# Kernel tuning notes

Measured on AMD Instinct MI355X. Metric: run time of the kernel, lower is better.

## Reference

```python
import jax, jax.numpy as jnp
import numpy as np

INPUT_DIM = 8192
HIDDEN = 512
EMBED = HIDDEN // 2  # op embedding dim
NUM_TEMPERS = 64
NUM_OPS = 3
MAX_HOPS = 4
B = 2048


def setup_inputs() -> dict:
    key = jax.random.key(0)
    ks = jax.random.split(key, 10)
    n = lambda k, shape: jax.random.normal(k, shape, jnp.float32)
    return {
        "x": n(ks[0], (B, INPUT_DIM)),
        "op_emb": 0.01 * n(ks[1], (NUM_OPS, EMBED)),
        "op_logits": jnp.zeros((NUM_OPS,), jnp.float32),
        "id_embeds": 0.01 * n(ks[2], (128, 4)),
        "W1": n(ks[3], (HIDDEN + 4 + EMBED, HIDDEN)) / np.sqrt(HIDDEN + 4 + EMBED),
        "b1": jnp.zeros((HIDDEN,), jnp.float32),
        "W2": n(ks[4], (HIDDEN, HIDDEN)) / np.sqrt(HIDDEN),
        "b2": jnp.zeros((HIDDEN,), jnp.float32),
        "Wr1": n(ks[5], (HIDDEN + 4, 32)) / np.sqrt(HIDDEN + 4),
        "br1": jnp.zeros((32,), jnp.float32),
        "Wr2": n(ks[6], (32, NUM_TEMPERS + 1)) / np.sqrt(32),
        "br2": jnp.zeros((NUM_TEMPERS + 1,), jnp.float32),
        "Wp": n(ks[7], (HIDDEN, INPUT_DIM)) / np.sqrt(HIDDEN),
        "bp": jnp.zeros((INPUT_DIM,), jnp.float32),
        "tid_emb": 0.01 * n(ks[8], (NUM_TEMPERS, 4)),
        "rng_seed": 42,
    }


def reference(x, op_emb, op_logits, id_embeds, W1, b1, W2, b2, Wr1, br1, Wr2, br2, Wp, bp, tid_emb, rng_seed):
    Bx, D = x.shape
    # D is a multiple of HIDDEN here -> no padding branch needed
    num_patches = D // HIDDEN
    patch_states = x.reshape(Bx * num_patches, HIDDEN)
    N = patch_states.shape[0]

    rng = jax.random.key(rng_seed)
    rng, tk = jax.random.split(rng)
    patch_tempers = jax.random.randint(tk, (N,), 0, NUM_TEMPERS)
    patch_done = jnp.zeros((N,), bool)

    # Fixed-length unroll of the while_loop (max_hops=4). Early-exit only
    # differs if ALL patches stop early, which is vanishingly unlikely.
    for hop in range(MAX_HOPS):
        # --- gather active patches (inactive slots fill with index 0, as in original) ---
        active_idx = jnp.where(~patch_done, size=N, fill_value=0)[0]
        x_active = patch_states[active_idx]          # [N, HIDDEN]
        t_active = patch_tempers[active_idx]         # [N]
        # --- Temper: sample op per patch, embed, 2-layer relu MLP ---
        rng, ok = jax.random.split(rng)
        op_probs = jax.nn.softmax(op_logits)
        op_idx = jax.random.categorical(ok, jnp.log(op_probs), shape=(N,))
        x_aug = jnp.concatenate([x_active, id_embeds[t_active], op_emb[op_idx]], axis=-1)
        h = jax.nn.relu(x_aug @ W1 + b1)
        h = jax.nn.relu(h @ W2 + b2)                 # [N, HIDDEN]
        # --- scatter back updated states ---
        patch_states = patch_states.at[active_idx].set(h)
        # --- routing policy + categorical sampling of next temper / stop ---
        enriched = jnp.concatenate([h, tid_emb[t_active]], axis=-1)
        logits = jax.nn.relu(enriched @ Wr1 + br1) @ Wr2 + br2
        rng, sk = jax.random.split(rng)
        sampled = jax.random.categorical(sk, jax.nn.log_softmax(logits))
        stop = sampled == NUM_TEMPERS
        next_t = jnp.clip(sampled, 0, NUM_TEMPERS - 1)
        patch_tempers = patch_tempers.at[active_idx].set(next_t)
        patch_done = patch_done.at[active_idx].set(stop)

    latent = patch_states.reshape(Bx, num_patches, HIDDEN).mean(axis=1)  # [B, HIDDEN]
    pred = latent @ Wp + bp                                              # [B, INPUT_DIM]
    return latent, pred
```

## Files before the change

kernel.cpp:

```cpp
#include <hip/hip_runtime.h>
#include <cstdint>
#include <cstddef>


#define NPATCH 32768
#define NHOP 4
#define RSCALE 4096.0f
#define RINV   2.44140625e-4f

typedef unsigned short u16;
typedef __attribute__((ext_vector_type(8))) _Float16 half8;
typedef __attribute__((ext_vector_type(4))) float f32x4;

#define GLDS(gp, lp) __builtin_amdgcn_global_load_lds( \
    (const __attribute__((address_space(1))) void*)(const void*)(gp), \
    (__attribute__((address_space(3))) void*)(void*)(lp), 16, 0, 0)

__device__ __forceinline__ uint32_t rotl32(uint32_t x, int r){ return (x<<r)|(x>>(32-r)); }

__device__ __forceinline__ void tf2x32(uint32_t k0, uint32_t k1, uint32_t x0, uint32_t x1,
                                       uint32_t& o0, uint32_t& o1){
  uint32_t k2 = k0 ^ k1 ^ 0x1BD11BDAu;
  x0 += k0; x1 += k1;
#define TFR(r) { x0 += x1; x1 = rotl32(x1,(r)); x1 ^= x0; }
  TFR(13) TFR(15) TFR(26) TFR(6)   x0 += k1; x1 += k2 + 1u;
  TFR(17) TFR(29) TFR(16) TFR(24)  x0 += k2; x1 += k0 + 2u;
  TFR(13) TFR(15) TFR(26) TFR(6)   x0 += k0; x1 += k1 + 3u;
  TFR(17) TFR(29) TFR(16) TFR(24)  x0 += k1; x1 += k2 + 4u;
  TFR(13) TFR(15) TFR(26) TFR(6)   x0 += k2; x1 += k0 + 5u;
#undef TFR
  o0 = x0; o1 = x1;
}

__device__ __forceinline__ uint32_t jbits32(uint32_t k0, uint32_t k1, uint32_t idx){
  uint32_t a, b; tf2x32(k0, k1, 0u, idx, a, b);
  return a ^ b;
}

__device__ __forceinline__ void jsplit(uint32_t& r0, uint32_t& r1, uint32_t& c0, uint32_t& c1){
  uint32_t n0, n1;
  tf2x32(r0, r1, 0u, 0u, n0, n1);
  tf2x32(r0, r1, 0u, 1u, c0, c1);
  r0 = n0; r1 = n1;
}

__device__ __forceinline__ float jgumbel(uint32_t bits){
  float f = __uint_as_float(0x3f800000u | (bits >> 9)) - 1.0f;
  float u = fmaxf(f, 1.17549435e-38f);
  return -logf(-logf(u));
}

union uhcv { _Float16 h; u16 u; };
__device__ __forceinline__ u16 f2h(float x){ uhcv t; t.h = (_Float16)x; return t.u; }
__device__ __forceinline__ float h2f(u16 b){ uhcv t; t.u = b; return (float)t.h; }
__device__ __forceinline__ void split2s(float v, u16& a0, u16& a1){
  a0 = f2h(v);
  a1 = f2h((v - h2f(a0)) * RSCALE);
}

__global__ void k_keys(const int* __restrict__ seed, const float* __restrict__ op_logits,
                       uint32_t* __restrict__ keys, float* __restrict__ logp3){
  if (threadIdx.x != 0 || blockIdx.x != 0) return;
  uint32_t r0 = 0u, r1 = (uint32_t)seed[0];
  uint32_t c0, c1;
  jsplit(r0, r1, c0, c1); keys[0] = c0; keys[1] = c1;
  for (int h = 0; h < NHOP; h++){
    jsplit(r0, r1, c0, c1); keys[2 + 4*h] = c0; keys[3 + 4*h] = c1;
    jsplit(r0, r1, c0, c1); keys[4 + 4*h] = c0; keys[5 + 4*h] = c1;
  }
  float l0 = op_logits[0], l1 = op_logits[1], l2 = op_logits[2];
  float mm = fmaxf(l0, fmaxf(l1, l2));
  float e0 = expf(l0-mm), e1 = expf(l1-mm), e2 = expf(l2-mm);
  float ssum = e0 + e1 + e2;
  logp3[0] = logf(e0/ssum); logp3[1] = logf(e1/ssum); logp3[2] = logf(e2/ssum);
}

__global__ __launch_bounds__(256)
void k_init(const uint32_t* __restrict__ keys, int* __restrict__ tempers, int* __restrict__ done){
  int i = blockIdx.x*256 + threadIdx.x;
  uint32_t b = jbits32(keys[0], keys[1], (uint32_t)(NPATCH + i));
  tempers[i] = (int)(b & 63u);
  done[i] = 0;
}

__global__ __launch_bounds__(256)
void k_precomp(const float* __restrict__ id_embeds, const float* __restrict__ op_emb,
               const float* __restrict__ tid_emb,
               const float* __restrict__ W1, const float* __restrict__ b1,
               const float* __restrict__ Wr1, const float* __restrict__ br1,
               float* __restrict__ idW, float* __restrict__ opWb, float* __restrict__ tidWb){
  int b = blockIdx.x, tid = threadIdx.x;
  if (b < 64){
    for (int j = tid; j < 512; j += 256){
      float v = 0.f;
      #pragma unroll
      for (int u = 0; u < 4; u++) v = fmaf(id_embeds[b*4+u], W1[(size_t)(512+u)*512 + j], v);
      idW[b*512 + j] = v;
    }
  } else if (b < 67){
    int o = b - 64;
    for (int j = tid; j < 512; j += 256){
      float v = b1[j];
      for (int u = 0; u < 256; u++) v = fmaf(op_emb[o*256+u], W1[(size_t)(516+u)*512 + j], v);
      opWb[o*512 + j] = v;
    }
  } else {
    for (int idx = tid; idx < 2048; idx += 256){
      int t = idx >> 5, c = idx & 31;
      float v = br1[c];
      #pragma unroll
      for (int u = 0; u < 4; u++) v = fmaf(tid_emb[t*4+u], Wr1[(512+u)*32 + c], v);
      tidWb[idx] = v;
    }
  }
}

__global__ __launch_bounds__(256)
void k_splitW(const float* __restrict__ W1, const float* __restrict__ W2,
              const float* __restrict__ Wp, const float* __restrict__ Wr1,
              u16* __restrict__ W1T, u16* __restrict__ W2T, u16* __restrict__ WpT,
              u16* __restrict__ Wr1P){
  __shared__ float t[32][33];
  int blk = blockIdx.x;
  const float* src; u16* dst; int N; int deg; size_t pst; int tb;
  if (blk < 256){ src = W1; dst = W1T; N = 512; deg = 2; pst = (size_t)512*512; tb = blk; }
  else if (blk < 512){ src = W2; dst = W2T; N = 512; deg = 2; pst = (size_t)512*512; tb = blk - 256; }
  else if (blk < 528){ src = Wr1; dst = Wr1P; N = 32; deg = 2; pst = (size_t)32*512; tb = blk - 512; }
  else { src = Wp; dst = WpT; N = 8192; deg = 1; pst = 0; tb = blk - 528; }
  int n0 = (tb >> 4)*32, k0 = (tb & 15)*32;
  if (N == 32){ n0 = 0; k0 = tb*32; }
  int r = threadIdx.x >> 5, c = threadIdx.x & 31;
  for (int rr = r; rr < 32; rr += 8)
    t[rr][c] = src[(size_t)(k0+rr)*N + ((n0 + c) % N)];
  __syncthreads();
  for (int rr = r; rr < 32; rr += 8){
    if (n0 + rr >= N) break;
    float v = t[c][rr];
    size_t o = (size_t)(n0+rr)*512 + k0 + c;
    if (deg == 2){
      u16 a0, a1; split2s(v, a0, a1);
      dst[o] = a0; dst[pst + o] = a1;
    } else {
      dst[o] = f2h(v);
    }
  }
}

__global__ __launch_bounds__(256)
void k_xsplit(const float* __restrict__ x, u16* __restrict__ sP){
  size_t i = ((size_t)blockIdx.x*256 + threadIdx.x)*4;
  float4 v = *(const float4*)(x + i);
  ushort4 p0, p1;
  split2s(v.x, p0.x, p1.x); split2s(v.y, p0.y, p1.y);
  split2s(v.z, p0.z, p1.z); split2s(v.w, p0.w, p1.w);
  const size_t SP = (size_t)NPATCH*512;
  *(ushort4*)(sP + i) = p0; *(ushort4*)(sP + SP + i) = p1;
}

__global__ __launch_bounds__(1024)
void k_scan1(const int* __restrict__ done, int* __restrict__ lpref,
             int* __restrict__ partials){
  __shared__ int cnt[1024];
  const int tid = threadIdx.x;
  const int e = blockIdx.x*1024 + tid;
  int f = (done[e] == 0);
  cnt[tid] = f;
  __syncthreads();
  int val = f;
  for (int off = 1; off < 1024; off <<= 1){
    int v = (tid >= off) ? cnt[tid - off] : 0;
    __syncthreads();
    val += v; cnt[tid] = val;
    __syncthreads();
  }
  lpref[e] = val - f;
  if (tid == 1023) partials[blockIdx.x] = val;
}

__global__ void k_scan2(int* __restrict__ partials, int* __restrict__ meta){
  const int tid = threadIdx.x;
  int f = (tid < 32) ? partials[tid] : 0;
  int v = f;
  #pragma unroll
  for (int off = 1; off < 32; off <<= 1){
    int u = __shfl_up(v, off);
    if (tid >= off) v += u;
  }
  if (tid < 32) partials[tid] = v - f;
  if (tid == 31){
    meta[0] = v;
    meta[1] = (v < NPATCH) ? (NPATCH - 1) : 0;
  }
}

__global__ __launch_bounds__(1024)
void k_scan3(const int* __restrict__ done, const int* __restrict__ lpref,
             const int* __restrict__ partials, const int* __restrict__ meta,
             const int* __restrict__ tempers,
             const uint32_t* __restrict__ keys, const float* __restrict__ logp3,
             int hop, int* __restrict__ aidx, int* __restrict__ t_act,
             int* __restrict__ op_idx){
  const int tid = threadIdx.x;
  const int e = blockIdx.x*1024 + tid;
  const int base = partials[blockIdx.x];
  const int lp = lpref[e];
  const int f = (done[e] == 0);
  const int na = meta[0];
  const int pos = f ? (base + lp) : (na + (e - base - lp));
  const int p = f ? e : 0;
  aidx[pos] = p;
  t_act[pos] = tempers[p];
  const uint32_t k0 = keys[2 + 4*hop], k1 = keys[3 + 4*hop];
  float best = 0.f; int bi = 0;
  #pragma unroll
  for (int c = 0; c < 3; c++){
    float v = jgumbel(jbits32(k0, k1, (uint32_t)(3*pos + c))) + logp3[c];
    if (c == 0 || v > best){ best = v; bi = c; }
  }
  op_idx[pos] = bi;
}

__global__ __launch_bounds__(1024)
void k_scan(const int* __restrict__ done, int* __restrict__ aidx, int* __restrict__ meta){
  __shared__ int cnt[1024];
  int tid = threadIdx.x;
  int base = tid * 32;
  unsigned flags = 0; int c = 0;
  #pragma unroll
  for (int i = 0; i < 32; i++){
    int f = (done[base + i] == 0);
    flags |= ((unsigned)f) << i;
    c += f;
  }
  cnt[tid] = c;
  __syncthreads();
  int val = c;
  for (int off = 1; off < 1024; off <<= 1){
    int v = (tid >= off) ? cnt[tid - off] : 0;
    __syncthreads();
    val += v; cnt[tid] = val;
    __syncthreads();
  }
  int pos = val - c;
  for (int i = 0; i < 32; i++){
    if ((flags >> i) & 1u) aidx[pos++] = base + i;
  }
  __syncthreads();
  int na = cnt[1023];
  for (int j = na + tid; j < NPATCH; j += 1024) aidx[j] = 0;
  if (tid == 0){
    meta[0] = na;
    meta[1] = (na < NPATCH) ? (NPATCH - 1) : 0;
  }
}

__global__ __launch_bounds__(256)
void k_gather(const int* __restrict__ aidx, const int* __restrict__ tempers,
              const uint32_t* __restrict__ keys, const float* __restrict__ logp3,
              int hop, int* __restrict__ t_act, int* __restrict__ op_idx){
  int s = blockIdx.x*256 + threadIdx.x;
  int p = aidx[s];
  t_act[s] = tempers[p];
  uint32_t k0 = keys[2 + 4*hop], k1 = keys[3 + 4*hop];
  float best = 0.f; int bi = 0;
  #pragma unroll
  for (int c = 0; c < 3; c++){
    float v = jgumbel(jbits32(k0, k1, (uint32_t)(3*s + c))) + logp3[c];
    if (c == 0 || v > best){ best = v; bi = c; }
  }
  op_idx[s] = bi;
}

template<int MODE, int DEG>
__global__ __launch_bounds__(256, 2)
void k_mgemm(const u16* __restrict__ Ap, const u16* __restrict__ Bp,
             float* __restrict__ outF, u16* __restrict__ outP,
             const int* __restrict__ aidx, const float* __restrict__ bias,
             const float* __restrict__ idW, const float* __restrict__ opWb,
             const int* __restrict__ t_act, const int* __restrict__ op_idx,
             const int* __restrict__ meta,
             int Ncols, size_t aStride, size_t bStride, size_t oStride){
  __shared__ u16 As[2*DEG*4096];
  __shared__ u16 Bs[2*DEG*4096];
  const int tid = threadIdx.x;
  const int L = tid & 63, w = tid >> 6;

  const int gx = (int)gridDim.x;
  const int nwg = gx * (int)gridDim.y;
  int lin = (int)blockIdx.y * gx + (int)blockIdx.x;
  if ((nwg & 7) == 0)
    lin = (lin & 7) * (nwg >> 3) + (lin >> 3);
  const int m0 = (lin / gx) * 128, n0 = (lin % gx) * 128;
  const int wr = w >> 1, wc = w & 1;

  constexpr int SPW = DEG*4;
  constexpr int BUFO = DEG*4096;
  const bool isA = (w < 2);
  const u16* gB = isA ? Ap : Bp;
  u16* lB = isA ? As : Bs;
  const size_t pstride = isA ? aStride : bStride;
  const u16* gseg[8];
  u16* lseg[8];
  #pragma unroll
  for (int q = 0; q < SPW; q++){
    int ss = (w & 1)*SPW + q;
    int p = ss >> 3, rb = ss & 7;
    int row16 = rb*16 + (L >> 2);
    int grow;
    if (isA) grow = (MODE == 1) ? aidx[m0 + row16] : (m0 + row16);
    else     grow = n0 + row16;
    int swz = (L & 3) ^ ((L >> 2) & 3);
    gseg[q] = gB + p*pstride + (size_t)grow*512 + swz*8;
    lseg[q] = lB + p*4096 + rb*512;
  }

  f32x4 accM[4][4], accR[4][4];
  #pragma unroll
  for (int i = 0; i < 4; i++)
    #pragma unroll
    for (int j = 0; j < 4; j++){ accM[i][j] = (f32x4)0.f; accR[i][j] = (f32x4)0.f; }

  const int rdsw = ((L >> 4) ^ (L & 3))*8;
  const int frow = L & 15;

  #pragma unroll
  for (int q = 0; q < SPW; q++)
    GLDS(gseg[q], lseg[q]);

  #pragma unroll 2
  for (int kt = 0; kt < 16; kt++){
    const int cb = (kt & 1) * BUFO;
    if (kt < 15){
      const int nb = ((kt + 1) & 1) * BUFO;
      #pragma unroll
      for (int q = 0; q < SPW; q++)
        GLDS(gseg[q] + (kt+1)*32, lseg[q] + nb);
      asm volatile("s_waitcnt vmcnt(%0)" :: "n"(SPW) : "memory");
    } else {
      asm volatile("s_waitcnt vmcnt(0)" ::: "memory");
    }
    __builtin_amdgcn_s_barrier();
    asm volatile("" ::: "memory");

    __builtin_amdgcn_s_setprio(1);
    #pragma unroll
    for (int pa = 0; pa < DEG; pa++){
      half8 af[4];
      #pragma unroll
      for (int i = 0; i < 4; i++)
        af[i] = *(const half8*)&As[cb + pa*4096 + (wr*64 + i*16 + frow)*32 + rdsw];
      #pragma unroll
      for (int pb = 0; pb < DEG - pa; pb++){
        #pragma unroll
        for (int j = 0; j < 4; j++){
          half8 bf = *(const half8*)&Bs[cb + pb*4096 + (wc*64 + j*16 + frow)*32 + rdsw];
          #pragma unroll
          for (int i = 0; i < 4; i++){
            if (pa + pb == 0)
              accM[i][j] = __builtin_amdgcn_mfma_f32_16x16x32_f16(af[i], bf, accM[i][j], 0, 0, 0);
            else
              accR[i][j] = __builtin_amdgcn_mfma_f32_16x16x32_f16(af[i], bf, accR[i][j], 0, 0, 0);
          }
        }
      }
    }
    __builtin_amdgcn_s_setprio(0);

    asm volatile("" ::: "memory");
    __builtin_amdgcn_s_barrier();
  }

  const int rbase = m0 + wr*64 + (L >> 4)*4;
  const int cbase = n0 + wc*64 + (L & 15);
  const int w0v = (MODE == 3) ? meta[1] : 0;
  #pragma unroll
  for (int i = 0; i < 4; i++){
    #pragma unroll
    for (int reg = 0; reg < 4; reg++){
      int r = rbase + i*16 + reg;
      if (MODE == 1){
        int t = t_act[r], o = op_idx[r];
        #pragma unroll
        for (int j = 0; j < 4; j++){
          int c = cbase + j*16;
          float v = accM[i][j][reg] + RINV*accR[i][j][reg] + idW[t*512 + c] + opWb[o*512 + c];
          v = fmaxf(v, 0.f);
          u16 a0, a1; split2s(v, a0, a1);
          size_t off = (size_t)r*512 + c;
          outP[off] = a0; outP[oStride + off] = a1;
        }
      } else if (MODE == 3){
        int p = aidx[r];
        bool allowed = (p != 0) || (r == w0v);
        #pragma unroll
        for (int j = 0; j < 4; j++){
          int c = cbase + j*16;
          float v = accM[i][j][reg] + RINV*accR[i][j][reg] + bias[c];
          v = fmaxf(v, 0.f);
          if (allowed){
            u16 a0, a1; split2s(v, a0, a1);
            size_t off = (size_t)p*512 + c;
            outP[off] = a0; outP[oStride + off] = a1;
          }
        }
      } else {
        #pragma unroll
        for (int j = 0; j < 4; j++){
          int c = cbase + j*16;
          float v = accM[i][j][reg] + bias[c];
          if (DEG == 2) v += RINV*accR[i][j][reg];
          outF[(size_t)r*Ncols + c] = v;
        }
      }
    }
  }
}

__global__ __launch_bounds__(256)
void k_routemm(const u16* __restrict__ sP, const u16* __restrict__ Wr1P,
               const int* __restrict__ aidx, const int* __restrict__ t_act,
               const float* __restrict__ tidWb, float* __restrict__ l32g){
  const int tid = threadIdx.x;
  const int L = tid & 63, w = tid >> 6;
  const int s0 = blockIdx.x*64 + w*16;
  const size_t SPh = (size_t)NPATCH*512;

  const int arow = aidx[s0 + (L & 15)];
  const u16* a0p = sP + (size_t)arow*512 + (L >> 4)*8;
  const u16* a1p = a0p + SPh;
  const u16* bb = Wr1P + (size_t)(L & 15)*512 + (L >> 4)*8;
  const size_t BPL = (size_t)32*512;
  const size_t BCT = (size_t)16*512;

  f32x4 accM[2], accR[2];
  accM[0] = (f32x4)0.f; accM[1] = (f32x4)0.f;
  accR[0] = (f32x4)0.f; accR[1] = (f32x4)0.f;

  #pragma unroll 4
  for (int kt = 0; kt < 16; kt++){
    const int ko = kt*32;
    half8 a0  = *(const half8*)(a0p + ko);
    half8 a1  = *(const half8*)(a1p + ko);
    half8 b00 = *(const half8*)(bb + ko);
    half8 b01 = *(const half8*)(bb + BCT + ko);
    half8 b10 = *(const half8*)(bb + BPL + ko);
    half8 b11 = *(const half8*)(bb + BPL + BCT + ko);
    accM[0] = __builtin_amdgcn_mfma_f32_16x16x32_f16(a0, b00, accM[0], 0, 0, 0);
    accM[1] = __builtin_amdgcn_mfma_f32_16x16x32_f16(a0, b01, accM[1], 0, 0, 0);
    accR[0] = __builtin_amdgcn_mfma_f32_16x16x32_f16(a0, b10, accR[0], 0, 0, 0);
    accR[1] = __builtin_amdgcn_mfma_f32_16x16x32_f16(a0, b11, accR[1], 0, 0, 0);
    accR[0] = __builtin_amdgcn_mfma_f32_16x16x32_f16(a1, b00, accR[0], 0, 0, 0);
    accR[1] = __builtin_amdgcn_mfma_f32_16x16x32_f16(a1, b01, accR[1], 0, 0, 0);
  }

  #pragma unroll
  for (int reg = 0; reg < 4; reg++){
    int s = s0 + (L >> 4)*4 + reg;
    int t = t_act[s];
    #pragma unroll
    for (int ct = 0; ct < 2; ct++){
      int c = ct*16 + (L & 15);
      float v = accM[ct][reg] + RINV*accR[ct][reg] + tidWb[t*32 + c];
      l32g[(size_t)s*32 + c] = fmaxf(v, 0.f);
    }
  }
}

__global__ __launch_bounds__(256)
void k_sample(const float* __restrict__ l32g, const float* __restrict__ Wr2,
              const float* __restrict__ br2,
              const int* __restrict__ aidx, const int* __restrict__ meta,
              const uint32_t* __restrict__ keys, int hop,
              int* __restrict__ tempers, int* __restrict__ done){
  __shared__ float l32s[8][32];
  __shared__ float Wr2s[32*65];
  const int tid = threadIdx.x;
  const int s0 = blockIdx.x * 8;
  l32s[tid >> 5][tid & 31] = l32g[(size_t)s0*32 + tid];
  for (int i = tid; i < 32*65; i += 256) Wr2s[i] = Wr2[i];
  __syncthreads();

  const int lane = tid & 63, w = tid >> 6;
  const int half = lane >> 5;
  const uint32_t sk0 = keys[4 + 4*hop], sk1 = keys[5 + 4*hop];
  int smp[2];
  for (int pass = 0; pass < 2; pass++){
    const int psl = w*2 + pass;
    const int ps  = s0 + psl;
    const int c = lane;
    float lg = br2[c];
    #pragma unroll
    for (int k = 0; k < 32; k++) lg = fmaf(l32s[psl][k], Wr2s[k*65 + c], lg);
    float lg64 = br2[64];
    #pragma unroll
    for (int k = 0; k < 32; k++) lg64 = fmaf(l32s[psl][k], Wr2s[k*65 + 64], lg64);
    float m = lg;
    for (int off = 32; off; off >>= 1) m = fmaxf(m, __shfl_xor(m, off));
    m = fmaxf(m, lg64);
    float se = expf(lg - m);
    for (int off = 32; off; off >>= 1) se += __shfl_xor(se, off);
    se += expf(lg64 - m);
    float Lse = logf(se);
    float g = jgumbel(jbits32(sk0, sk1, (uint32_t)(65*ps + c)));
    float v = (lg - m) - Lse + g;
    int idx = c;
    for (int off = 32; off; off >>= 1){
      float ov = __shfl_xor(v, off);
      int   oi = __shfl_xor(idx, off);
      if (ov > v || (ov == v && oi < idx)){ v = ov; idx = oi; }
    }
    float g64 = jgumbel(jbits32(sk0, sk1, (uint32_t)(65*ps + 64)));
    float v64 = (lg64 - m) - Lse + g64;
    if (v64 > v) idx = 64;
    smp[pass] = idx;
  }

  const int s = s0 + w*2 + half;
  const int mysmp = smp[half];
  const int p = aidx[s];
  const bool allowed = (p != 0) || (s == meta[1]);
  if (allowed && (lane & 31) == 0){
    tempers[p] = (mysmp < 63) ? mysmp : 63;
    done[p]    = (mysmp == 64) ? 1 : 0;
  }
}

__global__ __launch_bounds__(256)
void k_latent2(const u16* __restrict__ sP, float* __restrict__ outF, u16* __restrict__ latP){
  int idx = blockIdx.x*256 + threadIdx.x;
  int b = idx >> 9, j = idx & 511;
  const size_t SP = (size_t)NPATCH*512;
  float s = 0.f;
  #pragma unroll 4
  for (int u = 0; u < 16; u++){
    size_t e = (size_t)(b*16 + u)*512 + j;
    s += h2f(sP[e]) + RINV*h2f(sP[SP + e]);
  }
  s *= 0.0625f;
  outF[idx] = s;
  latP[idx] = f2h(s);
}

template<int MODE>
__global__ __launch_bounds__(256)
void k_gemmF(const float* __restrict__ A, const float* __restrict__ B, float* __restrict__ C,
             int Ncols,
             const int* __restrict__ aidx,
             const float* __restrict__ bias,
             const float* __restrict__ idW, const float* __restrict__ opWb,
             const int* __restrict__ t_act, const int* __restrict__ op_idx){
  __shared__ float As[16][128];
  __shared__ float Bs[16][128];
  const int tid = threadIdx.x;
  const int bx = blockIdx.x, by = blockIdx.y;
  const int tx = tid & 15, ty = tid >> 4;
  const int lr = tid >> 1, lhalf = tid & 1;
  const int srow = by*128 + lr;
  const int arow = (MODE == 1) ? aidx[srow] : srow;
  const float* Ap = A + (size_t)arow*512 + lhalf*8;
  const float* Bp = B + (size_t)(tid >> 4)*Ncols + bx*128 + (tid & 15)*8;

  float acc[8][8];
  #pragma unroll
  for (int i = 0; i < 8; i++)
    #pragma unroll
    for (int j = 0; j < 8; j++) acc[i][j] = 0.f;

  for (int kt = 0; kt < 512; kt += 16){
    float4 a0 = *(const float4*)(Ap + kt);
    float4 a1 = *(const float4*)(Ap + kt + 4);
    float4 g0 = *(const float4*)(Bp + (size_t)kt*Ncols);
    float4 g1 = *(const float4*)(Bp + (size_t)kt*Ncols + 4);
    __syncthreads();
    As[lhalf*8+0][lr] = a0.x; As[lhalf*8+1][lr] = a0.y;
    As[lhalf*8+2][lr] = a0.z; As[lhalf*8+3][lr] = a0.w;
    As[lhalf*8+4][lr] = a1.x; As[lhalf*8+5][lr] = a1.y;
    As[lhalf*8+6][lr] = a1.z; As[lhalf*8+7][lr] = a1.w;
    *(float4*)&Bs[tid>>4][(tid&15)*8]     = g0;
    *(float4*)&Bs[tid>>4][(tid&15)*8 + 4] = g1;
    __syncthreads();
    #pragma unroll
    for (int k = 0; k < 16; k++){
      float4 av0 = *(float4*)&As[k][ty*8];
      float4 av1 = *(float4*)&As[k][ty*8+4];
      float4 bv0 = *(float4*)&Bs[k][tx*4];
      float4 bv1 = *(float4*)&Bs[k][64 + tx*4];
      float av[8] = {av0.x,av0.y,av0.z,av0.w,av1.x,av1.y,av1.z,av1.w};
      float bv[8] = {bv0.x,bv0.y,bv0.z,bv0.w,bv1.x,bv1.y,bv1.z,bv1.w};
      #pragma unroll
      for (int i = 0; i < 8; i++)
        #pragma unroll
        for (int j = 0; j < 8; j++)
          acc[i][j] = fmaf(av[i], bv[j], acc[i][j]);
    }
  }

  const int col0a = bx*128 + tx*4;
  const int col0b = col0a + 64;
  #pragma unroll
  for (int i = 0; i < 8; i++){
    int s = by*128 + ty*8 + i;
    float adda[4], addb[4];
    if (MODE == 1){
      int t = t_act[s], o = op_idx[s];
      float4 ia = *(const float4*)&idW[t*512 + col0a];
      float4 ib = *(const float4*)&idW[t*512 + col0b];
      float4 oa = *(const float4*)&opWb[o*512 + col0a];
      float4 ob = *(const float4*)&opWb[o*512 + col0b];
      adda[0]=ia.x+oa.x; adda[1]=ia.y+oa.y; adda[2]=ia.z+oa.z; adda[3]=ia.w+oa.w;
      addb[0]=ib.x+ob.x; addb[1]=ib.y+ob.y; addb[2]=ib.z+ob.z; addb[3]=ib.w+ob.w;
    } else {
      float4 ba = *(const float4*)&bias[col0a];
      float4 bb = *(const float4*)&bias[col0b];
      adda[0]=ba.x; adda[1]=ba.y; adda[2]=ba.z; adda[3]=ba.w;
      addb[0]=bb.x; addb[1]=bb.y; addb[2]=bb.z; addb[3]=bb.w;
    }
    float4 va, vb;
    float* pa = &va.x; float* pb = &vb.x;
    #pragma unroll
    for (int j = 0; j < 4; j++){
      float v0 = acc[i][j]   + adda[j];
      float v1 = acc[i][j+4] + addb[j];
      if (MODE != 2){ v0 = fmaxf(v0, 0.f); v1 = fmaxf(v1, 0.f); }
      pa[j] = v0; pb[j] = v1;
    }
    *(float4*)(C + (size_t)s*Ncols + col0a) = va;
    *(float4*)(C + (size_t)s*Ncols + col0b) = vb;
  }
}

__global__ __launch_bounds__(256)
void k_routeF(const float* __restrict__ h2, const float* __restrict__ Wr1,
              const float* __restrict__ Wr2, const float* __restrict__ br2,
              const float* __restrict__ tidWb,
              const int* __restrict__ t_act, const int* __restrict__ aidx,
              const int* __restrict__ meta, const uint32_t* __restrict__ keys, int hop,
              float* __restrict__ states, int* __restrict__ tempers, int* __restrict__ done){
  __shared__ float Wr1s[256][32];
  __shared__ float h2s[8][512];
  __shared__ float l32[8][32];

  const int tid = threadIdx.x;
  const int s0 = blockIdx.x * 8;

  for (int i4 = tid; i4 < 8*128; i4 += 256){
    int sl = i4 >> 7, q = i4 & 127;
    *(float4*)&h2s[sl][q*4] = *(const float4*)&h2[(size_t)(s0+sl)*512 + q*4];
  }

  const int lane = tid & 63, w = tid >> 6;
  const int half = lane >> 5, col = lane & 31;
  const int sl = w*2 + half;
  const int s  = s0 + sl;
  const int t  = t_act[s];
  float acc = tidWb[t*32 + col];

  for (int kh = 0; kh < 2; kh++){
    __syncthreads();
    for (int idx = tid; idx < 256*32; idx += 256)
      Wr1s[idx >> 5][idx & 31] = Wr1[kh*8192 + idx];
    __syncthreads();
    const int kb = kh * 256;
    #pragma unroll 4
    for (int k4 = 0; k4 < 64; k4++){
      float4 hv = *(float4*)&h2s[sl][kb + k4*4];
      acc = fmaf(hv.x, Wr1s[k4*4+0][col], acc);
      acc = fmaf(hv.y, Wr1s[k4*4+1][col], acc);
      acc = fmaf(hv.z, Wr1s[k4*4+2][col], acc);
      acc = fmaf(hv.w, Wr1s[k4*4+3][col], acc);
    }
  }
  l32[sl][col] = fmaxf(acc, 0.f);
  __syncthreads();

  const uint32_t sk0 = keys[4 + 4*hop], sk1 = keys[5 + 4*hop];
  int smp[2];
  for (int pass = 0; pass < 2; pass++){
    const int psl = w*2 + pass;
    const int ps  = s0 + psl;
    const int c = lane;
    float lg = br2[c];
    #pragma unroll
    for (int k = 0; k < 32; k++) lg = fmaf(l32[psl][k], Wr2[k*65 + c], lg);
    float lg64 = br2[64];
    #pragma unroll
    for (int k = 0; k < 32; k++) lg64 = fmaf(l32[psl][k], Wr2[k*65 + 64], lg64);
    float m = lg;
    for (int off = 32; off; off >>= 1) m = fmaxf(m, __shfl_xor(m, off));
    m = fmaxf(m, lg64);
    float se = expf(lg - m);
    for (int off = 32; off; off >>= 1) se += __shfl_xor(se, off);
    se += expf(lg64 - m);
    float Lse = logf(se);
    float g = jgumbel(jbits32(sk0, sk1, (uint32_t)(65*ps + c)));
    float v = (lg - m) - Lse + g;
    int idx = c;
    for (int off = 32; off; off >>= 1){
      float ov = __shfl_xor(v, off);
      int   oi = __shfl_xor(idx, off);
      if (ov > v || (ov == v && oi < idx)){ v = ov; idx = oi; }
    }
    float g64 = jgumbel(jbits32(sk0, sk1, (uint32_t)(65*ps + 64)));
    float v64 = (lg64 - m) - Lse + g64;
    if (v64 > v) idx = 64;
    smp[pass] = idx;
  }

  const int mysmp = smp[half];
  const int p = aidx[s];
  const int w0v = meta[1];
  const bool allowed = (p != 0) || (s == w0v);
  if (allowed){
    const float4* src = (const float4*)&h2s[sl][0];
    float4* dst = (float4*)(states + (size_t)p*512);
    for (int q = col; q < 128; q += 32) dst[q] = src[q];
    if (col == 0){
      tempers[p] = (mysmp < 63) ? mysmp : 63;
      done[p]    = (mysmp == 64) ? 1 : 0;
    }
  }
}

__global__ __launch_bounds__(256)
void k_latentF(const float* __restrict__ states, float* __restrict__ out){
  int idx = blockIdx.x*256 + threadIdx.x;
  int b = idx >> 9, j = idx & 511;
  float s = 0.f;
  #pragma unroll
  for (int u = 0; u < 16; u++) s += states[(size_t)(b*16 + u)*512 + j];
  out[idx] = s * 0.0625f;
}

extern "C" void kernel_launch(void* const* d_in, const int* in_sizes, int n_in,
                              void* d_out, int out_size, void* d_ws, size_t ws_size,
                              hipStream_t stream) {
  (void)in_sizes; (void)n_in; (void)out_size;
  const float* x         = (const float*)d_in[0];
  const float* op_emb    = (const float*)d_in[1];
  const float* op_logits = (const float*)d_in[2];
  const float* id_embeds = (const float*)d_in[3];
  const float* W1        = (const float*)d_in[4];
  const float* b1        = (const float*)d_in[5];
  const float* W2        = (const float*)d_in[6];
  const float* b2        = (const float*)d_in[7];
  const float* Wr1       = (const float*)d_in[8];
  const float* br1       = (const float*)d_in[9];
  const float* Wr2       = (const float*)d_in[10];
  const float* br2       = (const float*)d_in[11];
  const float* Wp        = (const float*)d_in[12];
  const float* bp        = (const float*)d_in[13];
  const float* tid_emb   = (const float*)d_in[14];
  const int*   seed      = (const int*)d_in[15];
  float* out = (float*)d_out;

  char* w = (char*)d_ws;
  uint32_t* keys = (uint32_t*)w;
  float* logp3   = (float*)(w + 256);
  int*   meta    = (int*)(w + 512);
  int*   tempers = (int*)(w + 4096);
  int*   done    = tempers + NPATCH;
  int*   t_act   = done + NPATCH;
  int*   op_idx  = t_act + NPATCH;
  int*   aidx    = op_idx + NPATCH;
  int*   lpref   = aidx + NPATCH;
  float* idW     = (float*)(lpref + NPATCH);
  float* opWb    = idW + 64*512;
  float* tidWb   = opWb + 3*512;
  int*   partials= (int*)(tidWb + 2048);

  const size_t SPh = (size_t)NPATCH*512;
  u16* W1T     = (u16*)(w + (1u<<20));
  u16* W2T     = W1T + (size_t)2*512*512;
  u16* Wr1P    = W2T + (size_t)2*512*512;
  u16* WpT     = Wr1P + (size_t)2*32*512;
  u16* latP    = WpT + (size_t)8192*512;
  u16* statesP = latP + (size_t)2048*512;
  u16* h1P     = statesP + 2*SPh;
  float* l32g  = (float*)(h1P + 2*SPh);
  const size_t NEED = (size_t)((char*)(l32g + (size_t)NPATCH*32) - w);

  k_keys<<<1, 64, 0, stream>>>(seed, op_logits, keys, logp3);
  k_init<<<NPATCH/256, 256, 0, stream>>>(keys, tempers, done);
  k_precomp<<<68, 256, 0, stream>>>(id_embeds, op_emb, tid_emb, W1, b1, Wr1, br1,
                                    idW, opWb, tidWb);

  if (ws_size >= NEED){
    k_splitW<<<4624, 256, 0, stream>>>(W1, W2, Wp, Wr1, W1T, W2T, WpT, Wr1P);
    k_xsplit<<<(NPATCH*512/4)/256, 256, 0, stream>>>(x, statesP);

    for (int hop = 0; hop < NHOP; hop++){
      k_scan1<<<NPATCH/1024, 1024, 0, stream>>>(done, lpref, partials);
      k_scan2<<<1, 64, 0, stream>>>(partials, meta);
      k_scan3<<<NPATCH/1024, 1024, 0, stream>>>(done, lpref, partials, meta,
                                                tempers, keys, logp3, hop,
                                                aidx, t_act, op_idx);
      k_mgemm<1,2><<<dim3(4, NPATCH/128), 256, 0, stream>>>(
          statesP, W1T, nullptr, h1P, aidx, nullptr, idW, opWb, t_act, op_idx, meta,
          512, SPh, (size_t)512*512, SPh);
      k_mgemm<3,2><<<dim3(4, NPATCH/128), 256, 0, stream>>>(
          h1P, W2T, nullptr, statesP, aidx, b2, nullptr, nullptr, nullptr, nullptr, meta,
          512, SPh, (size_t)512*512, SPh);
      k_routemm<<<NPATCH/64, 256, 0, stream>>>(statesP, Wr1P, aidx, t_act, tidWb, l32g);
      k_sample<<<NPATCH/8, 256, 0, stream>>>(l32g, Wr2, br2, aidx, meta, keys, hop,
                                             tempers, done);
    }

    k_latent2<<<(2048*512)/256, 256, 0, stream>>>(statesP, out, latP);
    k_mgemm<2,1><<<dim3(64, 16), 256, 0, stream>>>(
        latP, WpT, out + 2048*512, nullptr, nullptr, bp, nullptr, nullptr, nullptr, nullptr,
        nullptr, 8192, (size_t)2048*512, (size_t)8192*512, 0);
  } else {
    const size_t BIG0 = 2u<<20;
    const size_t SB   = (size_t)NPATCH * 512 * sizeof(float);
    float *states, *h1, *h2;
    bool copy_states;
    if (ws_size >= BIG0 + 3*SB){
      states = (float*)(w + BIG0);
      h1     = (float*)(w + BIG0 + SB);
      h2     = (float*)(w + BIG0 + 2*SB);
      copy_states = true;
    } else {
      states = (float*)d_in[0];
      h1     = (float*)(w + BIG0);
      h2     = (float*)(w + BIG0 + SB);
      copy_states = false;
    }
    if (copy_states)
      hipMemcpyAsync(states, x, SB, hipMemcpyDeviceToDevice, stream);

    for (int hop = 0; hop < NHOP; hop++){
      k_scan<<<1, 1024, 0, stream>>>(done, aidx, meta);
      k_gather<<<NPATCH/256, 256, 0, stream>>>(aidx, tempers, keys, logp3, hop, t_act, op_idx);
      k_gemmF<1><<<dim3(4, NPATCH/128), 256, 0, stream>>>(states, W1, h1, 512,
                                      aidx, nullptr, idW, opWb, t_act, op_idx);
      k_gemmF<0><<<dim3(4, NPATCH/128), 256, 0, stream>>>(h1, W2, h2, 512,
                                      nullptr, b2, nullptr, nullptr, nullptr, nullptr);
      k_routeF<<<NPATCH/8, 256, 0, stream>>>(h2, Wr1, Wr2, br2, tidWb, t_act, aidx,
                                      meta, keys, hop, states, tempers, done);
    }

    k_latentF<<<(2048*512)/256, 256, 0, stream>>>(states, out);
    k_gemmF<2><<<dim3(8192/128, 2048/128), 256, 0, stream>>>(out, Wp, out + 2048*512, 8192,
                                      nullptr, bp, nullptr, nullptr, nullptr, nullptr);
  }
}
```

Measured before the change: 985.7 us.

## Fuse scan2 into scan3, fuse route sampling into routemm, vectorize latent

Folds the single-block partial-sum scan into every scan3 block, removing one launch per hop. Merges the sampling kernel into the routing GEMM, so the 32-wide hidden activations stay in shared memory instead of round-tripping through global memory. Restructures the GEMM inner loop to preload all A and B fragments before issuing MFMAs, which raises register use. Vectorizes the latent mean kernel to 4-wide loads and stores. Risks include the larger register footprint and the serialized 16-row sampling loop per wave.

After: 986.0 us. About the same (+0.0%).

```diff
diff --git a/kernel.cpp b/kernel.cpp
--- a/kernel.cpp
+++ b/kernel.cpp
@@ -177,35 +177,32 @@
   if (tid == 1023) partials[blockIdx.x] = val;
 }
 
-__global__ void k_scan2(int* __restrict__ partials, int* __restrict__ meta){
-  const int tid = threadIdx.x;
-  int f = (tid < 32) ? partials[tid] : 0;
-  int v = f;
-  #pragma unroll
-  for (int off = 1; off < 32; off <<= 1){
-    int u = __shfl_up(v, off);
-    if (tid >= off) v += u;
-  }
-  if (tid < 32) partials[tid] = v - f;
-  if (tid == 31){
-    meta[0] = v;
-    meta[1] = (v < NPATCH) ? (NPATCH - 1) : 0;
-  }
-}
-
 __global__ __launch_bounds__(1024)
 void k_scan3(const int* __restrict__ done, const int* __restrict__ lpref,
-             const int* __restrict__ partials, const int* __restrict__ meta,
+             const int* __restrict__ partials,
              const int* __restrict__ tempers,
              const uint32_t* __restrict__ keys, const float* __restrict__ logp3,
              int hop, int* __restrict__ aidx, int* __restrict__ t_act,
-             int* __restrict__ op_idx){
+             int* __restrict__ op_idx, int* __restrict__ meta){
+  __shared__ int sb[33];
   const int tid = threadIdx.x;
+  if (tid < 64){
+    int f = (tid < 32) ? partials[tid] : 0;
+    int v = f;
+    #pragma unroll
+    for (int off = 1; off < 32; off <<= 1){
+      int u = __shfl_up(v, off);
+      if (tid >= off) v += u;
+    }
+    if (tid < 32) sb[tid] = v - f;
+    if (tid == 31) sb[32] = v;
+  }
+  __syncthreads();
+  const int base = sb[blockIdx.x];
+  const int na = sb[32];
   const int e = blockIdx.x*1024 + tid;
-  const int base = partials[blockIdx.x];
   const int lp = lpref[e];
   const int f = (done[e] == 0);
-  const int na = meta[0];
   const int pos = f ? (base + lp) : (na + (e - base - lp));
   const int p = f ? e : 0;
   aidx[pos] = p;
@@ -218,6 +215,10 @@
     if (c == 0 || v > best){ best = v; bi = c; }
   }
   op_idx[pos] = bi;
+  if (blockIdx.x == 0 && tid == 0){
+    meta[0] = na;
+    meta[1] = (na < NPATCH) ? (NPATCH - 1) : 0;
+  }
 }
 
 __global__ __launch_bounds__(1024)
@@ -343,27 +344,30 @@
     asm volatile("" ::: "memory");
 
     __builtin_amdgcn_s_setprio(1);
-    #pragma unroll
-    for (int pa = 0; pa < DEG; pa++){
-      half8 af[4];
+    half8 af[DEG][4], bf[DEG][4];
+    #pragma unroll
+    for (int pa = 0; pa < DEG; pa++)
       #pragma unroll
       for (int i = 0; i < 4; i++)
-        af[i] = *(const half8*)&As[cb + pa*4096 + (wr*64 + i*16 + frow)*32 + rdsw];
+        af[pa][i] = *(const half8*)&As[cb + pa*4096 + (wr*64 + i*16 + frow)*32 + rdsw];
+    #pragma unroll
+    for (int pb = 0; pb < DEG; pb++)
       #pragma unroll
-      for (int pb = 0; pb < DEG - pa; pb++){
+      for (int j = 0; j < 4; j++)
+        bf[pb][j] = *(const half8*)&Bs[cb + pb*4096 + (wc*64 + j*16 + frow)*32 + rdsw];
+    #pragma unroll
+    for (int pa = 0; pa < DEG; pa++)
+      #pragma unroll
+      for (int pb = 0; pb < DEG - pa; pb++)
         #pragma unroll
-        for (int j = 0; j < 4; j++){
-          half8 bf = *(const half8*)&Bs[cb + pb*4096 + (wc*64 + j*16 + frow)*32 + rdsw];
+        for (int j = 0; j < 4; j++)
           #pragma unroll
           for (int i = 0; i < 4; i++){
             if (pa + pb == 0)
-              accM[i][j] = __builtin_amdgcn_mfma_f32_16x16x32_f16(af[i], bf, accM[i][j], 0, 0, 0);
+              accM[i][j] = __builtin_amdgcn_mfma_f32_16x16x32_f16(af[0][i], bf[0][j], accM[i][j], 0, 0, 0);
             else
-              accR[i][j] = __builtin_amdgcn_mfma_f32_16x16x32_f16(af[i], bf, accR[i][j], 0, 0, 0);
+              accR[i][j] = __builtin_amdgcn_mfma_f32_16x16x32_f16(af[pa][i], bf[pb][j], accR[i][j], 0, 0, 0);
           }
-        }
-      }
-    }
     __builtin_amdgcn_s_setprio(0);
 
     asm volatile("" ::: "memory");
@@ -419,11 +423,18 @@
 __global__ __launch_bounds__(256)
 void k_routemm(const u16* __restrict__ sP, const u16* __restrict__ Wr1P,
                const int* __restrict__ aidx, const int* __restrict__ t_act,
-               const float* __restrict__ tidWb, float* __restrict__ l32g){
+               const float* __restrict__ tidWb,
+               const float* __restrict__ Wr2, const float* __restrict__ br2,
+               const int* __restrict__ meta, const uint32_t* __restrict__ keys,
+               int hop, int* __restrict__ tempers, int* __restrict__ done){
+  __shared__ float l32s[64][32];
+  __shared__ float Wr2s[32*65];
   const int tid = threadIdx.x;
   const int L = tid & 63, w = tid >> 6;
   const int s0 = blockIdx.x*64 + w*16;
   const size_t SPh = (size_t)NPATCH*512;
+
+  for (int i = tid; i < 32*65; i += 256) Wr2s[i] = Wr2[i];
 
   const int arow = aidx[s0 + (L & 15)];
   const u16* a0p = sP + (size_t)arow*512 + (L >> 4)*8;
@@ -455,45 +466,30 @@
 
   #pragma unroll
   for (int reg = 0; reg < 4; reg++){
-    int s = s0 + (L >> 4)*4 + reg;
+    int sl = w*16 + (L >> 4)*4 + reg;
+    int s = blockIdx.x*64 + sl;
     int t = t_act[s];
     #pragma unroll
     for (int ct = 0; ct < 2; ct++){
       int c = ct*16 + (L & 15);
       float v = accM[ct][reg] + RINV*accR[ct][reg] + tidWb[t*32 + c];
-      l32g[(size_t)s*32 + c] = fmaxf(v, 0.f);
-    }
-  }
-}
-
-__global__ __launch_bounds__(256)
-void k_sample(const float* __restrict__ l32g, const float* __restrict__ Wr2,
-              const float* __restrict__ br2,
-              const int* __restrict__ aidx, const int* __restrict__ meta,
-              const uint32_t* __restrict__ keys, int hop,
-              int* __restrict__ tempers, int* __restrict__ done){
-  __shared__ float l32s[8][32];
-  __shared__ float Wr2s[32*65];
-  const int tid = threadIdx.x;
-  const int s0 = blockIdx.x * 8;
-  l32s[tid >> 5][tid & 31] = l32g[(size_t)s0*32 + tid];
-  for (int i = tid; i < 32*65; i += 256) Wr2s[i] = Wr2[i];
+      l32s[sl][c] = fmaxf(v, 0.f);
+    }
+  }
   __syncthreads();
 
-  const int lane = tid & 63, w = tid >> 6;
-  const int half = lane >> 5;
   const uint32_t sk0 = keys[4 + 4*hop], sk1 = keys[5 + 4*hop];
-  int smp[2];
-  for (int pass = 0; pass < 2; pass++){
-    const int psl = w*2 + pass;
-    const int ps  = s0 + psl;
-    const int c = lane;
+  const int w0v = meta[1];
+  for (int rr = 0; rr < 16; rr++){
+    const int sl = w*16 + rr;
+    const int ps = blockIdx.x*64 + sl;
+    const int c = L;
     float lg = br2[c];
     #pragma unroll
-    for (int k = 0; k < 32; k++) lg = fmaf(l32s[psl][k], Wr2s[k*65 + c], lg);
+    for (int k = 0; k < 32; k++) lg = fmaf(l32s[sl][k], Wr2s[k*65 + c], lg);
     float lg64 = br2[64];
     #pragma unroll
-    for (int k = 0; k < 32; k++) lg64 = fmaf(l32s[psl][k], Wr2s[k*65 + 64], lg64);
+    for (int k = 0; k < 32; k++) lg64 = fmaf(l32s[sl][k], Wr2s[k*65 + 64], lg64);
     float m = lg;
     for (int off = 32; off; off >>= 1) m = fmaxf(m, __shfl_xor(m, off));
     m = fmaxf(m, lg64);
@@ -512,33 +508,38 @@
     float g64 = jgumbel(jbits32(sk0, sk1, (uint32_t)(65*ps + 64)));
     float v64 = (lg64 - m) - Lse + g64;
     if (v64 > v) idx = 64;
-    smp[pass] = idx;
-  }
-
-  const int s = s0 + w*2 + half;
-  const int mysmp = smp[half];
-  const int p = aidx[s];
-  const bool allowed = (p != 0) || (s == meta[1]);
-  if (allowed && (lane & 31) == 0){
-    tempers[p] = (mysmp < 63) ? mysmp : 63;
-    done[p]    = (mysmp == 64) ? 1 : 0;
+    if (L == 0){
+      const int p = aidx[ps];
+      const bool allowed = (p != 0) || (ps == w0v);
+      if (allowed){
+        tempers[p] = (idx < 63) ? idx : 63;
+        done[p]    = (idx == 64) ? 1 : 0;
+      }
+    }
   }
 }
 
 __global__ __launch_bounds__(256)
 void k_latent2(const u16* __restrict__ sP, float* __restrict__ outF, u16* __restrict__ latP){
   int idx = blockIdx.x*256 + threadIdx.x;
-  int b = idx >> 9, j = idx & 511;
+  int b = idx >> 7, j4 = (idx & 127)*4;
   const size_t SP = (size_t)NPATCH*512;
-  float s = 0.f;
+  float s0 = 0.f, s1 = 0.f, s2 = 0.f, s3 = 0.f;
   #pragma unroll 4
   for (int u = 0; u < 16; u++){
-    size_t e = (size_t)(b*16 + u)*512 + j;
-    s += h2f(sP[e]) + RINV*h2f(sP[SP + e]);
-  }
-  s *= 0.0625f;
-  outF[idx] = s;
-  latP[idx] = f2h(s);
+    size_t e = (size_t)(b*16 + u)*512 + j4;
+    ushort4 v0 = *(const ushort4*)(sP + e);
+    ushort4 v1 = *(const ushort4*)(sP + SP + e);
+    s0 += h2f(v0.x) + RINV*h2f(v1.x);
+    s1 += h2f(v0.y) + RINV*h2f(v1.y);
+    s2 += h2f(v0.z) + RINV*h2f(v1.z);
+    s3 += h2f(v0.w) + RINV*h2f(v1.w);
+  }
+  s0 *= 0.0625f; s1 *= 0.0625f; s2 *= 0.0625f; s3 *= 0.0625f;
+  float4 fo; fo.x = s0; fo.y = s1; fo.z = s2; fo.w = s3;
+  *(float4*)(outF + (size_t)b*512 + j4) = fo;
+  ushort4 lp; lp.x = f2h(s0); lp.y = f2h(s1); lp.z = f2h(s2); lp.w = f2h(s3);
+  *(ushort4*)(latP + (size_t)b*512 + j4) = lp;
 }
 
 template<int MODE>
@@ -776,8 +777,7 @@
   u16* latP    = WpT + (size_t)8192*512;
   u16* statesP = latP + (size_t)2048*512;
   u16* h1P     = statesP + 2*SPh;
-  float* l32g  = (float*)(h1P + 2*SPh);
-  const size_t NEED = (size_t)((char*)(l32g + (size_t)NPATCH*32) - w);
+  const size_t NEED = (size_t)((char*)(h1P + 2*SPh) - w);
 
   k_keys<<<1, 64, 0, stream>>>(seed, op_logits, keys, logp3);
   k_init<<<NPATCH/256, 256, 0, stream>>>(keys, tempers, done);
@@ -790,22 +790,21 @@
 
     for (int hop = 0; hop < NHOP; hop++){
       k_scan1<<<NPATCH/1024, 1024, 0, stream>>>(done, lpref, partials);
-      k_scan2<<<1, 64, 0, stream>>>(partials, meta);
-      k_scan3<<<NPATCH/1024, 1024, 0, stream>>>(done, lpref, partials, meta,
+      k_scan3<<<NPATCH/1024, 1024, 0, stream>>>(done, lpref, partials,
                                                 tempers, keys, logp3, hop,
-                                                aidx, t_act, op_idx);
+                                                aidx, t_act, op_idx, meta);
       k_mgemm<1,2><<<dim3(4, NPATCH/128), 256, 0, stream>>>(
           statesP, W1T, nullptr, h1P, aidx, nullptr, idW, opWb, t_act, op_idx, meta,
           512, SPh, (size_t)512*512, SPh);
       k_mgemm<3,2><<<dim3(4, NPATCH/128), 256, 0, stream>>>(
           h1P, W2T, nullptr, statesP, aidx, b2, nullptr, nullptr, nullptr, nullptr, meta,
           512, SPh, (size_t)512*512, SPh);
-      k_routemm<<<NPATCH/64, 256, 0, stream>>>(statesP, Wr1P, aidx, t_act, tidWb, l32g);
-      k_sample<<<NPATCH/8, 256, 0, stream>>>(l32g, Wr2, br2, aidx, meta, keys, hop,
-                                             tempers, done);
-    }
-
-    k_latent2<<<(2048*512)/256, 256, 0, stream>>>(statesP, out, latP);
+      k_routemm<<<NPATCH/64, 256, 0, stream>>>(statesP, Wr1P, aidx, t_act, tidWb,
+                                               Wr2, br2, meta, keys, hop,
+                                               tempers, done);
+    }
+
+    k_latent2<<<(2048*512/4)/256, 256, 0, stream>>>(statesP, out, latP);
     k_mgemm<2,1><<<dim3(64, 16), 256, 0, stream>>>(
         latP, WpT, out + 2048*512, nullptr, nullptr, bp, nullptr, nullptr, nullptr, nullptr,
         nullptr, 8192, (size_t)2048*512, (size_t)8192*512, 0);
```
